# Optimization experiments

Measured on AMD Instinct MI355X. Metric: run time of the kernel, lower is better.

## Reference

```python
import jax, jax.numpy as jnp
import numpy as np

B = 32768
NUM_CLASS = 1000
FEATURE_DIM = 512


def setup_inputs() -> dict:
    key = jax.random.key(0)
    k1, k2, k3 = jax.random.split(key, 3)
    features = jax.random.normal(k1, (B, FEATURE_DIM), dtype=jnp.float32)
    labels = jax.random.randint(k2, (B,), 0, NUM_CLASS, dtype=jnp.int32)
    center = jax.random.normal(k3, (NUM_CLASS, FEATURE_DIM), dtype=jnp.float32)
    return {"features": features, "labels": labels, "center": center}


def reference(features, labels, center):
    C = center.shape[0]
    # ---- intra loss: per-row euclidean distance to own-class center ----
    # (equivalent to gathering dist_mat[i, labels[i]] from cdist(features, center, p=2))
    diff = features - center[labels]                      # [B, D]
    dist = jnp.sqrt(jnp.sum(diff * diff, axis=-1))        # [B]
    dist = jnp.clip(dist, 1e-12, 1e12)
    intra_loss = dist.mean()

    # ---- inter loss ----
    # torch: center.scatter_add(0, labels_rep, features) -> center_param + per-class sum
    sums = jax.ops.segment_sum(features, labels, num_segments=C)          # [C, D]
    # counts: scatter_add with index [B,1] only uses first column of ones -> class counts
    counts = jax.ops.segment_sum(jnp.ones((features.shape[0],), features.dtype),
                                 labels, num_segments=C)                  # [C]
    cen = (center + sums) / jnp.clip(counts, 1.0, None)[:, None]          # [C, D]
    # source bug: loop keeps only the LAST combination (C-2, C-1)
    d_last = jnp.sqrt(jnp.sum((cen[C - 2] - cen[C - 1]) ** 2))
    inter_loss = (2.0 / d_last) * (1.0 / (C * (C - 1)))
    return (intra_loss, inter_loss)
```

## Files before the change

### kernel.cpp

```cpp
#include <hip/hip_runtime.h>

#define B_ROWS   32768
#define NUM_CLS  1000
#define FEAT     512

#define BLOCKS          4096
#define THREADS         256
#define WAVES_PER_BLOCK 4
#define ROWS_PER_WAVE   2

typedef float f32x4 __attribute__((ext_vector_type(4)));

#define WS_CNT0   1
#define WS_CNT1   2
#define WS_SUM0   64
#define WS_SUM1   (64 + 512)
#define WS_PART   (64 + 1024)
#define WS_ZERO_FLOATS (64 + 1024)

__global__ __launch_bounds__(THREADS) void loss_pass1(
    const float* __restrict__ features,
    const int*   __restrict__ labels,
    const float* __restrict__ center,
    float*       __restrict__ ws)
{
    const int wave = threadIdx.x >> 6;
    const int lane = threadIdx.x & 63;
    const int wid  = blockIdx.x * WAVES_PER_BLOCK + wave;
    const int base_row = wid * ROWS_PER_WAVE;

    const int mylab = labels[base_row + (lane & 1)];

    f32x4 f[4], c[4];
    #pragma unroll
    for (int r = 0; r < ROWS_PER_WAVE; ++r) {
        const f32x4* frow = (const f32x4*)(features + (size_t)(base_row + r) * FEAT);
        f[2*r]     = frow[lane];
        f[2*r + 1] = frow[lane + 64];
    }
    #pragma unroll
    for (int r = 0; r < ROWS_PER_WAVE; ++r) {
        const int lab = __shfl(mylab, r);
        const f32x4* crow = (const f32x4*)(center + (size_t)lab * FEAT);
        c[2*r]     = crow[lane];
        c[2*r + 1] = crow[lane + 64];
    }

    float p[ROWS_PER_WAVE];
    #pragma unroll
    for (int r = 0; r < ROWS_PER_WAVE; ++r) {
        f32x4 d0 = f[2*r]     - c[2*r];
        f32x4 d1 = f[2*r + 1] - c[2*r + 1];
        p[r] = d0.x*d0.x + d0.y*d0.y + d0.z*d0.z + d0.w*d0.w
             + d1.x*d1.x + d1.y*d1.y + d1.z*d1.z + d1.w*d1.w;
    }

    #pragma unroll
    for (int r = 0; r < ROWS_PER_WAVE; ++r) {
        const int lab = __shfl(mylab, r);
        if (lab >= NUM_CLS - 2) {
            float* sums = ws + (lab == NUM_CLS - 2 ? WS_SUM0 : WS_SUM1);
            const int base = lane * 4;
            f32x4 f0 = f[2*r], f1 = f[2*r + 1];
            atomicAdd(&sums[base + 0],   f0.x);
            atomicAdd(&sums[base + 1],   f0.y);
            atomicAdd(&sums[base + 2],   f0.z);
            atomicAdd(&sums[base + 3],   f0.w);
            atomicAdd(&sums[base + 256], f1.x);
            atomicAdd(&sums[base + 257], f1.y);
            atomicAdd(&sums[base + 258], f1.z);
            atomicAdd(&sums[base + 259], f1.w);
            if (lane == 0)
                atomicAdd(&ws[lab == NUM_CLS - 2 ? WS_CNT0 : WS_CNT1], 1.0f);
        }
    }

    const bool b0 = lane & 1;
    float send = b0 ? p[0] : p[1];
    float keep = b0 ? p[1] : p[0];
    float u = keep + __shfl_xor(send, 1);
    u += __shfl_xor(u, 2);
    u += __shfl_xor(u, 4);
    u += __shfl_xor(u, 8);
    u += __shfl_xor(u, 16);
    u += __shfl_xor(u, 32);
    float dist = sqrtf(u);
    dist = fminf(fmaxf(dist, 1e-12f), 1e12f);
    dist += __shfl_xor(dist, 1);
    const float acc = dist;

    __shared__ float s[WAVES_PER_BLOCK];
    if (lane == 0) s[wave] = acc;
    __syncthreads();
    if (threadIdx.x == 0)
        ws[WS_PART + blockIdx.x] = s[0] + s[1] + s[2] + s[3];
}

__global__ __launch_bounds__(256) void loss_pass2(
    const float* __restrict__ center,
    const float* __restrict__ ws,
    float*       __restrict__ out)
{
    const int t = threadIdx.x;
    const float cnt0 = fmaxf(ws[WS_CNT0], 1.0f);
    const float cnt1 = fmaxf(ws[WS_CNT1], 1.0f);

    float p_inter = 0.0f;
    #pragma unroll
    for (int k = 0; k < 2; ++k) {
        const int d = t * 2 + k;
        float a = (center[(size_t)(NUM_CLS - 2) * FEAT + d] + ws[WS_SUM0 + d]) / cnt0;
        float b = (center[(size_t)(NUM_CLS - 1) * FEAT + d] + ws[WS_SUM1 + d]) / cnt1;
        float df = a - b;
        p_inter += df * df;
    }

    const f32x4* part4 = (const f32x4*)(ws + WS_PART);
    float p_intra = 0.0f;
    #pragma unroll
    for (int k = 0; k < 4; ++k) {
        f32x4 v = part4[t + k * 256];
        p_intra += (v.x + v.y) + (v.z + v.w);
    }

    #pragma unroll
    for (int off = 32; off; off >>= 1) {
        p_inter += __shfl_xor(p_inter, off);
        p_intra += __shfl_xor(p_intra, off);
    }

    __shared__ float si[4], sa[4];
    if ((t & 63) == 0) { si[t >> 6] = p_inter; sa[t >> 6] = p_intra; }
    __syncthreads();

    if (t == 0) {
        float d_last = sqrtf(si[0] + si[1] + si[2] + si[3]);
        out[0] = (sa[0] + sa[1] + sa[2] + sa[3]) * (1.0f / (float)B_ROWS);
        out[1] = (2.0f / d_last) * (1.0f / ((float)NUM_CLS * (float)(NUM_CLS - 1)));
    }
}

extern "C" void kernel_launch(void* const* d_in, const int* in_sizes, int n_in,
                              void* d_out, int out_size, void* d_ws, size_t ws_size,
                              hipStream_t stream) {
    const float* features = (const float*)d_in[0];
    const int*   labels   = (const int*)d_in[1];
    const float* center   = (const float*)d_in[2];
    float* out = (float*)d_out;
    float* ws  = (float*)d_ws;

    (void)hipMemsetAsync(ws, 0, WS_ZERO_FLOATS * sizeof(float), stream);

    loss_pass1<<<BLOCKS, THREADS, 0, stream>>>(features, labels, center, ws);
    loss_pass2<<<1, 256, 0, stream>>>(center, ws, out);
}
```

Before: 25.42 us.

## Replace global atomics with dedicated inter-loss blocks and drop workspace memset

Adds 16 extra blocks that each scan a slice of labels, build a shared-memory list of rows belonging to the last two classes, and write per-block partial sums and counts to private slots. Pass 2 reduces these slots. This removes global float atomics from the intra-loss blocks and the hipMemsetAsync launch, since every slot is now overwritten instead of accumulated. It risks silently dropping rows if a slice holds more than 128 matching labels (expected about 66 per slice), and the inter blocks re-read feature rows.

```diff
diff --git a/kernel.cpp b/kernel.cpp
--- a/kernel.cpp
+++ b/kernel.cpp
@@ -4,19 +4,19 @@
 #define NUM_CLS  1000
 #define FEAT     512
 
-#define BLOCKS          4096
+#define INTER_BLOCKS    16
+#define INTRA_BLOCKS    4096
 #define THREADS         256
 #define WAVES_PER_BLOCK 4
 #define ROWS_PER_WAVE   2
+#define LABELS_PER_IB   (B_ROWS / INTER_BLOCKS)
+#define LISTCAP         128
 
 typedef float f32x4 __attribute__((ext_vector_type(4)));
+typedef float f32x2 __attribute__((ext_vector_type(2)));
 
-#define WS_CNT0   1
-#define WS_CNT1   2
-#define WS_SUM0   64
-#define WS_SUM1   (64 + 512)
-#define WS_PART   (64 + 1024)
-#define WS_ZERO_FLOATS (64 + 1024)
+#define WS_INTER 4096
+#define SLOT     1032
 
 __global__ __launch_bounds__(THREADS) void loss_pass1(
     const float* __restrict__ features,
@@ -24,9 +24,52 @@
     const float* __restrict__ center,
     float*       __restrict__ ws)
 {
+    if (blockIdx.x < INTER_BLOCKS) {
+        const int ib = blockIdx.x;
+        const int t  = threadIdx.x;
+
+        __shared__ int list[LISTCAP];
+        __shared__ int nm_s;
+        if (t == 0) nm_s = 0;
+        __syncthreads();
+
+        const int4* lab4 = (const int4*)(labels + ib * LABELS_PER_IB);
+        #pragma unroll
+        for (int k = 0; k < 2; ++k) {
+            const int j = t + k * 256;
+            int4 L = lab4[j];
+            const int row0 = ib * LABELS_PER_IB + 4 * j;
+            if (L.x >= NUM_CLS - 2) { int i = atomicAdd(&nm_s, 1); if (i < LISTCAP) list[i] = (row0 << 1)       | (L.x - (NUM_CLS - 2)); }
+            if (L.y >= NUM_CLS - 2) { int i = atomicAdd(&nm_s, 1); if (i < LISTCAP) list[i] = ((row0 + 1) << 1) | (L.y - (NUM_CLS - 2)); }
+            if (L.z >= NUM_CLS - 2) { int i = atomicAdd(&nm_s, 1); if (i < LISTCAP) list[i] = ((row0 + 2) << 1) | (L.z - (NUM_CLS - 2)); }
+            if (L.w >= NUM_CLS - 2) { int i = atomicAdd(&nm_s, 1); if (i < LISTCAP) list[i] = ((row0 + 3) << 1) | (L.w - (NUM_CLS - 2)); }
+        }
+        __syncthreads();
+        const int nm = min(nm_s, LISTCAP);
+
+        float s0a = 0.0f, s0b = 0.0f, s1a = 0.0f, s1b = 0.0f;
+        int c0 = 0, c1 = 0;
+        for (int m = 0; m < nm; ++m) {
+            const int e   = list[m];
+            const int row = e >> 1;
+            const f32x2 v = ((const f32x2*)(features + (size_t)row * FEAT))[t];
+            if (e & 1) { s1a += v.x; s1b += v.y; ++c1; }
+            else       { s0a += v.x; s0b += v.y; ++c0; }
+        }
+
+        float* slot = ws + WS_INTER + ib * SLOT;
+        if (t == 0) { slot[0] = (float)c0; slot[1] = (float)c1; }
+        f32x2 v0; v0.x = s0a; v0.y = s0b;
+        f32x2 v1; v1.x = s1a; v1.y = s1b;
+        ((f32x2*)(slot + 2))[t]   = v0;
+        ((f32x2*)(slot + 514))[t] = v1;
+        return;
+    }
+
+    const int bid  = blockIdx.x - INTER_BLOCKS;
     const int wave = threadIdx.x >> 6;
     const int lane = threadIdx.x & 63;
-    const int wid  = blockIdx.x * WAVES_PER_BLOCK + wave;
+    const int wid  = bid * WAVES_PER_BLOCK + wave;
     const int base_row = wid * ROWS_PER_WAVE;
 
     const int mylab = labels[base_row + (lane & 1)];
@@ -55,26 +98,6 @@
              + d1.x*d1.x + d1.y*d1.y + d1.z*d1.z + d1.w*d1.w;
     }
 
-    #pragma unroll
-    for (int r = 0; r < ROWS_PER_WAVE; ++r) {
-        const int lab = __shfl(mylab, r);
-        if (lab >= NUM_CLS - 2) {
-            float* sums = ws + (lab == NUM_CLS - 2 ? WS_SUM0 : WS_SUM1);
-            const int base = lane * 4;
-            f32x4 f0 = f[2*r], f1 = f[2*r + 1];
-            atomicAdd(&sums[base + 0],   f0.x);
-            atomicAdd(&sums[base + 1],   f0.y);
-            atomicAdd(&sums[base + 2],   f0.z);
-            atomicAdd(&sums[base + 3],   f0.w);
-            atomicAdd(&sums[base + 256], f1.x);
-            atomicAdd(&sums[base + 257], f1.y);
-            atomicAdd(&sums[base + 258], f1.z);
-            atomicAdd(&sums[base + 259], f1.w);
-            if (lane == 0)
-                atomicAdd(&ws[lab == NUM_CLS - 2 ? WS_CNT0 : WS_CNT1], 1.0f);
-        }
-    }
-
     const bool b0 = lane & 1;
     float send = b0 ? p[0] : p[1];
     float keep = b0 ? p[1] : p[0];
@@ -87,13 +110,12 @@
     float dist = sqrtf(u);
     dist = fminf(fmaxf(dist, 1e-12f), 1e12f);
     dist += __shfl_xor(dist, 1);
-    const float acc = dist;
 
     __shared__ float s[WAVES_PER_BLOCK];
-    if (lane == 0) s[wave] = acc;
+    if (lane == 0) s[wave] = dist;
     __syncthreads();
     if (threadIdx.x == 0)
-        ws[WS_PART + blockIdx.x] = s[0] + s[1] + s[2] + s[3];
+        ws[bid] = s[0] + s[1] + s[2] + s[3];
 }
 
 __global__ __launch_bounds__(256) void loss_pass2(
@@ -102,20 +124,36 @@
     float*       __restrict__ out)
 {
     const int t = threadIdx.x;
-    const float cnt0 = fmaxf(ws[WS_CNT0], 1.0f);
-    const float cnt1 = fmaxf(ws[WS_CNT1], 1.0f);
 
-    float p_inter = 0.0f;
+    float cnt0 = 0.0f, cnt1 = 0.0f;
     #pragma unroll
-    for (int k = 0; k < 2; ++k) {
-        const int d = t * 2 + k;
-        float a = (center[(size_t)(NUM_CLS - 2) * FEAT + d] + ws[WS_SUM0 + d]) / cnt0;
-        float b = (center[(size_t)(NUM_CLS - 1) * FEAT + d] + ws[WS_SUM1 + d]) / cnt1;
-        float df = a - b;
-        p_inter += df * df;
+    for (int b = 0; b < INTER_BLOCKS; ++b) {
+        const float* slot = ws + WS_INTER + b * SLOT;
+        cnt0 += slot[0];
+        cnt1 += slot[1];
+    }
+    cnt0 = fmaxf(cnt0, 1.0f);
+    cnt1 = fmaxf(cnt1, 1.0f);
+
+    float s0a = 0.0f, s0b = 0.0f, s1a = 0.0f, s1b = 0.0f;
+    #pragma unroll
+    for (int b = 0; b < INTER_BLOCKS; ++b) {
+        const float* slot = ws + WS_INTER + b * SLOT;
+        f32x2 v0 = ((const f32x2*)(slot + 2))[t];
+        f32x2 v1 = ((const f32x2*)(slot + 514))[t];
+        s0a += v0.x; s0b += v0.y;
+        s1a += v1.x; s1b += v1.y;
     }
 
-    const f32x4* part4 = (const f32x4*)(ws + WS_PART);
+    const int d = 2 * t;
+    float a0 = (center[(size_t)(NUM_CLS - 2) * FEAT + d]     + s0a) / cnt0;
+    float b0 = (center[(size_t)(NUM_CLS - 1) * FEAT + d]     + s1a) / cnt1;
+    float a1 = (center[(size_t)(NUM_CLS - 2) * FEAT + d + 1] + s0b) / cnt0;
+    float b1 = (center[(size_t)(NUM_CLS - 1) * FEAT + d + 1] + s1b) / cnt1;
+    float df0 = a0 - b0, df1 = a1 - b1;
+    float p_inter = df0 * df0 + df1 * df1;
+
+    const f32x4* part4 = (const f32x4*)ws;
     float p_intra = 0.0f;
     #pragma unroll
     for (int k = 0; k < 4; ++k) {
@@ -149,8 +187,6 @@
     float* out = (float*)d_out;
     float* ws  = (float*)d_ws;
 
-    (void)hipMemsetAsync(ws, 0, WS_ZERO_FLOATS * sizeof(float), stream);
-
-    loss_pass1<<<BLOCKS, THREADS, 0, stream>>>(features, labels, center, ws);
+    loss_pass1<<<INTER_BLOCKS + INTRA_BLOCKS, THREADS, 0, stream>>>(features, labels, center, ws);
     loss_pass2<<<1, 256, 0, stream>>>(center, ws, out);
 }
```

New measurement: 21.69 us. 1.17x faster.
